# Optimization experiments

Hardware: AMD Instinct MI355X
Metric: run time of the kernel (lower is better)

Reference implementation:

```python
import jax, jax.numpy as jnp
import numpy as np

B, T, K_LAB = 32, 2048, 256
MASK = 1.0  # scalar mask blend coefficient from __init__ (1.0 = no padding)


def setup_inputs() -> dict:
    key = jax.random.key(0)
    k1, k2, k3 = jax.random.split(key, 3)
    y_pred = jax.random.normal(k1, (B, T, K_LAB), dtype=jnp.float32)  # emissions
    labels = jax.random.randint(k2, (B, T), 0, K_LAB, dtype=jnp.int32)  # gold tag ids
    # crf_trans weight, keras 'uniform' initializer ~ U(-0.05, 0.05)
    trans = jax.random.uniform(k3, (K_LAB, K_LAB), dtype=jnp.float32, minval=-0.05, maxval=0.05)
    return {"y_pred": y_pred, "trans": trans, "labels": labels}


def reference(y_pred, trans, labels):
    K = y_pred.shape[-1]
    y_true = jax.nn.one_hot(labels, K, dtype=y_pred.dtype)  # [B,T,K]

    # ---- path_score (unnormalized log prob of gold path) ----
    point_score = jnp.sum(y_pred * y_true, axis=(1, 2))[:, None]  # [B,1]
    # original materializes [B,T-1,K,K]; einsum computes the same contraction
    trans_score = jnp.einsum('bti,ij,btj->b', y_true[:, :-1], trans, y_true[:, 1:])[:, None]
    path_score = point_score + trans_score  # [B,1]

    # ---- log partition via forward algorithm (log-sum-exp semiring scan) ----
    init = y_pred[:, 0]  # [B,K]

    def step(state, x_t):
        # state: [B,K] alpha_{t-1};  x_t: [B,K] emissions at t
        new = jax.nn.logsumexp(state[:, :, None] + trans[None, :, :], axis=1) + x_t
        new = MASK * new + (1.0 - MASK) * state  # mask blend (identity for MASK=1)
        return new, None

    xs = jnp.swapaxes(y_pred[:, 1:], 0, 1)  # [T-1,B,K]
    final, _ = jax.lax.scan(step, init, xs)
    log_norm = jax.nn.logsumexp(final, axis=1, keepdims=True)  # [B,1]

    return log_norm - path_score  # [B,1] negative log-likelihood
```

## Files before the change

### kernel.cpp

```cpp
#include <hip/hip_runtime.h>

#define B_N 32
#define T_N 2048
#define K_N 256

typedef _Float16 f16x8 __attribute__((ext_vector_type(8)));
typedef float f32x4 __attribute__((ext_vector_type(4)));

#define LN2x5 3.46573590280f
#define C_ALL 7097.82712893f

__global__ __launch_bounds__(256) void k_rowmax(const float* __restrict__ y,
                                                float* __restrict__ mx) {
  int row = blockIdx.x * 4 + (threadIdx.x >> 6);
  int l = threadIdx.x & 63;
  const float4* p = (const float4*)(y + (size_t)row * K_N);
  float4 v = p[l];
  float m = fmaxf(fmaxf(v.x, v.y), fmaxf(v.z, v.w));
#pragma unroll
  for (int s = 1; s < 64; s <<= 1) m = fmaxf(m, __shfl_xor(m, s));
  if (l == 0) mx[row] = m;
}

__global__ __launch_bounds__(256) void k_expT(const float* __restrict__ trans,
                                              _Float16* __restrict__ ET) {
  int i = blockIdx.x;
  int j = threadIdx.x;
  ET[j * K_N + i] = (_Float16)__expf(trans[i * K_N + j]);
}

__global__ __launch_bounds__(256) void k_scores(
    const float* __restrict__ y, const int* __restrict__ lab,
    const float* __restrict__ trans, const float* __restrict__ mx,
    float* __restrict__ smx, float* __restrict__ path) {
  const int b = blockIdx.x;
  const int tid = threadIdx.x;
  float s_mx = 0.f, s_pt = 0.f, s_tr = 0.f;
  for (int t = tid; t < T_N; t += 256) {
    s_mx += mx[b * T_N + t];
    int lt = lab[b * T_N + t];
    s_pt += y[((size_t)b * T_N + t) * K_N + lt];
    if (t < T_N - 1) {
      int lnx = lab[b * T_N + t + 1];
      s_tr += trans[lt * K_N + lnx];
    }
  }
#pragma unroll
  for (int s = 1; s < 64; s <<= 1) {
    s_mx += __shfl_xor(s_mx, s);
    s_pt += __shfl_xor(s_pt, s);
    s_tr += __shfl_xor(s_tr, s);
  }
  __shared__ float r0[4], r1[4], r2[4];
  int w = tid >> 6, l = tid & 63;
  if (l == 0) { r0[w] = s_mx; r1[w] = s_pt; r2[w] = s_tr; }
  __syncthreads();
  if (tid == 0) {
    smx[b] = r0[0] + r0[1] + r0[2] + r0[3];
    path[b] = (r1[0] + r1[1] + r1[2] + r1[3]) + (r2[0] + r2[1] + r2[2] + r2[3]);
  }
}

__global__ __launch_bounds__(256, 1) void k_crf(
    const float* __restrict__ y, const _Float16* __restrict__ ET,
    const float* __restrict__ mx, const float* __restrict__ smx,
    const float* __restrict__ path, float* __restrict__ out) {
  const int b = blockIdx.x;
  const int tid = threadIdx.x;
  const int w = tid >> 6;
  const int l = tid & 63;
  const int lr = l & 15;
  const int lg = (l >> 4) & 3;

  alignas(16) __shared__ _Float16 vbuf[2][K_N];
  alignas(16) __shared__ float red[4];

  const float* __restrict__ yb = y + (size_t)b * T_N * K_N + w * 64 + lr;
  const float* __restrict__ mxb = mx + b * T_N;

  f16x8 E0[8], E1[8], E2[8], E3[8];
  {
    const f16x8* ETv = (const f16x8*)ET;
#pragma unroll
    for (int kt = 0; kt < 8; ++kt) {
      E0[kt] = ETv[(w * 64 + 0 * 16 + lr) * 32 + kt * 4 + lg];
      E1[kt] = ETv[(w * 64 + 1 * 16 + lr) * 32 + kt * 4 + lg];
      E2[kt] = ETv[(w * 64 + 2 * 16 + lr) * 32 + kt * 4 + lg];
      E3[kt] = ETv[(w * 64 + 3 * 16 + lr) * 32 + kt * 4 + lg];
    }
  }

  {
    float m0 = mxb[0];
    float yv = y[(size_t)b * T_N * K_N + w * 64 + lg * 16 + lr];
    vbuf[0][w * 64 + lg * 16 + lr] = (_Float16)__expf(yv - m0 - LN2x5);
  }

  float ys[4][4];
  float mxs[4];
#define PREF(P, TT) { int tp_ = (TT); tp_ = tp_ > (T_N - 1) ? (T_N - 1) : tp_; \
    const float* yp_ = yb + (size_t)tp_ * K_N;                                 \
    ys[P][0] = yp_[0];  ys[P][1] = yp_[16];                                    \
    ys[P][2] = yp_[32]; ys[P][3] = yp_[48];                                    \
    mxs[P] = mxb[tp_]; }

  PREF(0, 1) PREF(1, 2) PREF(2, 3) PREF(3, 4)

  float Cn = 0.0f;
  float wv0 = 0.f, wv1 = 0.f, wv2 = 0.f, wv3 = 0.f;

#define BARRIER asm volatile("s_waitcnt lgkmcnt(0)\ns_barrier" ::: "memory");

  BARRIER

#define STEP(TT, P, RB, WB, RENORM, APPLY, DO_STORE, DO_PREF, DO_BAR) {        \
    const f16x8* vv_ = (const f16x8*)&vbuf[RB][0];                             \
    f16x8 A_[8];                                                               \
    _Pragma("unroll")                                                          \
    for (int kt = 0; kt < 8; ++kt) A_[kt] = vv_[kt * 4 + lg];                  \
    float bias_ = mxs[P] + LN2x5;                                              \
    if (APPLY) {                                                               \
      f32x4 rv_ = *(const f32x4*)red;                                          \
      float mR_ = fmaxf(fmaxf(rv_[0], rv_[1]), fmaxf(rv_[2], rv_[3]));         \
      float lm_ = __logf(mR_);                                                 \
      Cn += lm_; bias_ += lm_;                                                 \
    }                                                                          \
    float e0_ = __expf(ys[P][0] - bias_);                                      \
    float e1_ = __expf(ys[P][1] - bias_);                                      \
    float e2_ = __expf(ys[P][2] - bias_);                                      \
    float e3_ = __expf(ys[P][3] - bias_);                                      \
    if (DO_PREF) PREF(P, (TT) + 4)                                             \
    f32x4 a0_ = {0.f, 0.f, 0.f, 0.f};                                          \
    f32x4 a1_ = a0_, a2_ = a0_, a3_ = a0_;                                     \
    _Pragma("unroll")                                                          \
    for (int kt = 0; kt < 8; ++kt) {                                           \
      a0_ = __builtin_amdgcn_mfma_f32_16x16x32_f16(A_[kt], E0[kt], a0_, 0, 0, 0); \
      a1_ = __builtin_amdgcn_mfma_f32_16x16x32_f16(A_[kt], E1[kt], a1_, 0, 0, 0); \
      a2_ = __builtin_amdgcn_mfma_f32_16x16x32_f16(A_[kt], E2[kt], a2_, 0, 0, 0); \
      a3_ = __builtin_amdgcn_mfma_f32_16x16x32_f16(A_[kt], E3[kt], a3_, 0, 0, 0); \
    }                                                                          \
    wv0 = a0_[0] * e0_; wv1 = a1_[0] * e1_;                                    \
    wv2 = a2_[0] * e2_; wv3 = a3_[0] * e3_;                                    \
    if (RENORM) {                                                              \
      float ml_ = fmaxf(fmaxf(wv0, wv1), fmaxf(wv2, wv3));                     \
      ml_ = fmaxf(ml_, __shfl_xor(ml_, 1));                                    \
      ml_ = fmaxf(ml_, __shfl_xor(ml_, 2));                                    \
      ml_ = fmaxf(ml_, __shfl_xor(ml_, 4));                                    \
      ml_ = fmaxf(ml_, __shfl_xor(ml_, 8));                                    \
      if (l == 0) red[w] = ml_;                                                \
    }                                                                          \
    if (DO_STORE) {                                                            \
      float sv_ = lg == 0 ? wv0 : lg == 1 ? wv1 : lg == 2 ? wv2 : wv3;         \
      vbuf[WB][w * 64 + lg * 16 + lr] = (_Float16)sv_;                         \
    }                                                                          \
    if (DO_BAR) BARRIER                                                        \
  }

  STEP(1, 0, 0, 1, 0, 0, 1, 1, 1)
  STEP(2, 1, 1, 0, 0, 0, 1, 1, 1)
  STEP(3, 2, 0, 1, 0, 0, 1, 1, 1)
  STEP(4, 3, 1, 0, 1, 0, 1, 1, 1)

#pragma unroll 1
  for (int t0 = 5; t0 <= T_N - 7; t0 += 4) {
    STEP(t0,     0, 0, 1, 0, 1, 1, 1, 1)
    STEP(t0 + 1, 1, 1, 0, 0, 0, 1, 1, 1)
    STEP(t0 + 2, 2, 0, 1, 0, 0, 1, 1, 1)
    STEP(t0 + 3, 3, 1, 0, 1, 0, 1, 1, 1)
  }

  STEP(2045, 0, 0, 1, 0, 1, 1, 0, 1)
  STEP(2046, 1, 1, 0, 0, 0, 1, 0, 1)
  STEP(2047, 2, 0, 1, 0, 0, 0, 0, 0)

  float s = wv0 + wv1 + wv2 + wv3;
  s += __shfl_xor(s, 1);
  s += __shfl_xor(s, 2);
  s += __shfl_xor(s, 4);
  s += __shfl_xor(s, 8);
  if (l == 0) red[w] = s;
  BARRIER
  if (tid == 0) {
    float S = red[0] + red[1] + red[2] + red[3];
    out[b] = __logf(S) + Cn + smx[b] + C_ALL - path[b];
  }
}

extern "C" void kernel_launch(void* const* d_in, const int* in_sizes, int n_in,
                              void* d_out, int out_size, void* d_ws, size_t ws_size,
                              hipStream_t stream) {
  const float* y = (const float*)d_in[0];
  const float* trans = (const float*)d_in[1];
  const int* lab = (const int*)d_in[2];
  float* out = (float*)d_out;

  float* mx = (float*)d_ws;
  _Float16* ET = (_Float16*)((char*)d_ws + (size_t)B_N * T_N * 4);
  float* smx = (float*)((char*)d_ws + (size_t)B_N * T_N * 4 + (size_t)K_N * K_N * 2);
  float* path = smx + B_N;

  k_rowmax<<<dim3(B_N * T_N / 4), dim3(256), 0, stream>>>(y, mx);
  k_expT<<<dim3(K_N), dim3(K_N), 0, stream>>>(trans, ET);
  k_scores<<<dim3(B_N), dim3(256), 0, stream>>>(y, lab, trans, mx, smx, path);
  k_crf<<<dim3(B_N), dim3(256), 0, stream>>>(y, ET, mx, smx, path, out);
}
```

Before: 1.134 ms.

## Use FP8 scaled MFMA with exp(trans)-1 decomposition and per-step sum normalization

The forward recursion now runs in FP8. The transition matrix is stored as exp(trans)-1 in FP8 and the state vector is kept in FP8 in shared memory, so each 16-column tile needs only two 16x16x128 f8f6f4 MFMAs instead of eight f16 MFMAs. The dominant 1 term is added back exactly through the previous-step sum (Sp + a), which preserves accuracy for small transition values. Renormalisation moves from a periodic max to a per-step sum with a log every step, which adds a shuffle reduction and a logf to every iteration of the serial critical path.

```diff
diff --git a/kernel.cpp b/kernel.cpp
--- a/kernel.cpp
+++ b/kernel.cpp
@@ -4,11 +4,11 @@
 #define T_N 2048
 #define K_N 256
 
-typedef _Float16 f16x8 __attribute__((ext_vector_type(8)));
 typedef float f32x4 __attribute__((ext_vector_type(4)));
+typedef int i32x8 __attribute__((ext_vector_type(8)));
 
-#define LN2x5 3.46573590280f
-#define C_ALL 7097.82712893f
+#define MFMA8(A, B, C) \
+  __builtin_amdgcn_mfma_scale_f32_16x16x128_f8f6f4((A), (B), (C), 0, 0, 0, 0x7F7F7F7F, 0, 0x7F7F7F7F)
 
 __global__ __launch_bounds__(256) void k_rowmax(const float* __restrict__ y,
                                                 float* __restrict__ mx) {
@@ -22,11 +22,13 @@
   if (l == 0) mx[row] = m;
 }
 
-__global__ __launch_bounds__(256) void k_expT(const float* __restrict__ trans,
-                                              _Float16* __restrict__ ET) {
-  int i = blockIdx.x;
-  int j = threadIdx.x;
-  ET[j * K_N + i] = (_Float16)__expf(trans[i * K_N + j]);
+__global__ __launch_bounds__(256) void k_g8(const float* __restrict__ trans,
+                                            unsigned char* __restrict__ GT) {
+  int j = blockIdx.x;
+  int i = threadIdx.x;
+  float g = __expf(trans[i * K_N + j]) - 1.0f;
+  int pk = __builtin_amdgcn_cvt_pk_fp8_f32(g, 0.f, 0, false);
+  GT[j * K_N + i] = (unsigned char)(pk & 0xff);
 }
 
 __global__ __launch_bounds__(256) void k_scores(
@@ -62,7 +64,7 @@
 }
 
 __global__ __launch_bounds__(256, 1) void k_crf(
-    const float* __restrict__ y, const _Float16* __restrict__ ET,
+    const float* __restrict__ y, const unsigned char* __restrict__ GT,
     const float* __restrict__ mx, const float* __restrict__ smx,
     const float* __restrict__ path, float* __restrict__ out) {
   const int b = blockIdx.x;
@@ -72,28 +74,29 @@
   const int lr = l & 15;
   const int lg = (l >> 4) & 3;
 
-  alignas(16) __shared__ _Float16 vbuf[2][K_N];
-  alignas(16) __shared__ float red[4];
+  alignas(64) __shared__ unsigned char vbuf8[2][K_N];
+  alignas(16) __shared__ float red2[2][4];
 
   const float* __restrict__ yb = y + (size_t)b * T_N * K_N + w * 64 + lr;
   const float* __restrict__ mxb = mx + b * T_N;
 
-  f16x8 E0[8], E1[8], E2[8], E3[8];
-  {
-    const f16x8* ETv = (const f16x8*)ET;
+  i32x8 Bf[4][2];
 #pragma unroll
-    for (int kt = 0; kt < 8; ++kt) {
-      E0[kt] = ETv[(w * 64 + 0 * 16 + lr) * 32 + kt * 4 + lg];
-      E1[kt] = ETv[(w * 64 + 1 * 16 + lr) * 32 + kt * 4 + lg];
-      E2[kt] = ETv[(w * 64 + 2 * 16 + lr) * 32 + kt * 4 + lg];
-      E3[kt] = ETv[(w * 64 + 3 * 16 + lr) * 32 + kt * 4 + lg];
-    }
+  for (int tt = 0; tt < 4; ++tt) {
+#pragma unroll
+    for (int h = 0; h < 2; ++h)
+      Bf[tt][h] = *(const i32x8*)(GT + (size_t)(w * 64 + tt * 16 + lr) * K_N + h * 128 + lg * 32);
   }
 
   {
-    float m0 = mxb[0];
-    float yv = y[(size_t)b * T_N * K_N + w * 64 + lg * 16 + lr];
-    vbuf[0][w * 64 + lg * 16 + lr] = (_Float16)__expf(yv - m0 - LN2x5);
+    int c0 = w * 64 + lg * 16 + lr;
+    float v0 = __expf(y[(size_t)b * T_N * K_N + c0] - mxb[0]);
+    int pk = __builtin_amdgcn_cvt_pk_fp8_f32(v0, 0.f, 0, false);
+    vbuf8[0][c0] = (unsigned char)(pk & 0xff);
+    float ps = v0;
+#pragma unroll
+    for (int s = 1; s < 64; s <<= 1) ps += __shfl_xor(ps, s);
+    if (l == 0) red2[0][w] = ps;
   }
 
   float ys[4][4];
@@ -113,76 +116,56 @@
 
   BARRIER
 
-#define STEP(TT, P, RB, WB, RENORM, APPLY, DO_STORE, DO_PREF, DO_BAR) {        \
-    const f16x8* vv_ = (const f16x8*)&vbuf[RB][0];                             \
-    f16x8 A_[8];                                                               \
-    _Pragma("unroll")                                                          \
-    for (int kt = 0; kt < 8; ++kt) A_[kt] = vv_[kt * 4 + lg];                  \
-    float bias_ = mxs[P] + LN2x5;                                              \
-    if (APPLY) {                                                               \
-      f32x4 rv_ = *(const f32x4*)red;                                          \
-      float mR_ = fmaxf(fmaxf(rv_[0], rv_[1]), fmaxf(rv_[2], rv_[3]));         \
-      float lm_ = __logf(mR_);                                                 \
-      Cn += lm_; bias_ += lm_;                                                 \
-    }                                                                          \
+#define STEP(TT, P, RB, WB, DO_PREF) {                                         \
+    f32x4 r_ = *(const f32x4*)(&red2[((TT) - 1) & 1][0]);                      \
+    i32x8 A0_ = *(const i32x8*)(&vbuf8[RB][lg * 32]);                          \
+    i32x8 A1_ = *(const i32x8*)(&vbuf8[RB][128 + lg * 32]);                    \
+    float Sp_ = (r_[0] + r_[1]) + (r_[2] + r_[3]);                             \
+    float ls_ = __logf(Sp_);                                                   \
+    float bias_ = mxs[P] + ls_;                                                \
     float e0_ = __expf(ys[P][0] - bias_);                                      \
     float e1_ = __expf(ys[P][1] - bias_);                                      \
     float e2_ = __expf(ys[P][2] - bias_);                                      \
     float e3_ = __expf(ys[P][3] - bias_);                                      \
     if (DO_PREF) PREF(P, (TT) + 4)                                             \
-    f32x4 a0_ = {0.f, 0.f, 0.f, 0.f};                                          \
-    f32x4 a1_ = a0_, a2_ = a0_, a3_ = a0_;                                     \
-    _Pragma("unroll")                                                          \
-    for (int kt = 0; kt < 8; ++kt) {                                           \
-      a0_ = __builtin_amdgcn_mfma_f32_16x16x32_f16(A_[kt], E0[kt], a0_, 0, 0, 0); \
-      a1_ = __builtin_amdgcn_mfma_f32_16x16x32_f16(A_[kt], E1[kt], a1_, 0, 0, 0); \
-      a2_ = __builtin_amdgcn_mfma_f32_16x16x32_f16(A_[kt], E2[kt], a2_, 0, 0, 0); \
-      a3_ = __builtin_amdgcn_mfma_f32_16x16x32_f16(A_[kt], E3[kt], a3_, 0, 0, 0); \
+    f32x4 z_ = {0.f, 0.f, 0.f, 0.f};                                           \
+    f32x4 a0_ = MFMA8(A1_, Bf[0][1], MFMA8(A0_, Bf[0][0], z_));                \
+    f32x4 a1_ = MFMA8(A1_, Bf[1][1], MFMA8(A0_, Bf[1][0], z_));                \
+    f32x4 a2_ = MFMA8(A1_, Bf[2][1], MFMA8(A0_, Bf[2][0], z_));                \
+    f32x4 a3_ = MFMA8(A1_, Bf[3][1], MFMA8(A0_, Bf[3][0], z_));                \
+    wv0 = (Sp_ + a0_[0]) * e0_;                                                \
+    wv1 = (Sp_ + a1_[0]) * e1_;                                                \
+    wv2 = (Sp_ + a2_[0]) * e2_;                                                \
+    wv3 = (Sp_ + a3_[0]) * e3_;                                                \
+    Cn += ls_;                                                                 \
+    float ps_ = (wv0 + wv1) + (wv2 + wv3);                                     \
+    ps_ += __shfl_xor(ps_, 1);                                                 \
+    ps_ += __shfl_xor(ps_, 2);                                                 \
+    ps_ += __shfl_xor(ps_, 4);                                                 \
+    ps_ += __shfl_xor(ps_, 8);                                                 \
+    if (l == 0) red2[(TT) & 1][w] = ps_;                                       \
+    {                                                                          \
+      float sv_ = lg == 0 ? wv0 : lg == 1 ? wv1 : lg == 2 ? wv2 : wv3;         \
+      int pk_ = __builtin_amdgcn_cvt_pk_fp8_f32(sv_, 0.f, 0, false);           \
+      vbuf8[WB][w * 64 + lg * 16 + lr] = (unsigned char)(pk_ & 0xff);          \
     }                                                                          \
-    wv0 = a0_[0] * e0_; wv1 = a1_[0] * e1_;                                    \
-    wv2 = a2_[0] * e2_; wv3 = a3_[0] * e3_;                                    \
-    if (RENORM) {                                                              \
-      float ml_ = fmaxf(fmaxf(wv0, wv1), fmaxf(wv2, wv3));                     \
-      ml_ = fmaxf(ml_, __shfl_xor(ml_, 1));                                    \
-      ml_ = fmaxf(ml_, __shfl_xor(ml_, 2));                                    \
-      ml_ = fmaxf(ml_, __shfl_xor(ml_, 4));                                    \
-      ml_ = fmaxf(ml_, __shfl_xor(ml_, 8));                                    \
-      if (l == 0) red[w] = ml_;                                                \
-    }                                                                          \
-    if (DO_STORE) {                                                            \
-      float sv_ = lg == 0 ? wv0 : lg == 1 ? wv1 : lg == 2 ? wv2 : wv3;         \
-      vbuf[WB][w * 64 + lg * 16 + lr] = (_Float16)sv_;                         \
-    }                                                                          \
-    if (DO_BAR) BARRIER                                                        \
+    BARRIER                                                                    \
   }
 
-  STEP(1, 0, 0, 1, 0, 0, 1, 1, 1)
-  STEP(2, 1, 1, 0, 0, 0, 1, 1, 1)
-  STEP(3, 2, 0, 1, 0, 0, 1, 1, 1)
-  STEP(4, 3, 1, 0, 1, 0, 1, 1, 1)
+#pragma unroll 1
+  for (int t0 = 1; t0 <= T_N - 7; t0 += 4) {
+    STEP(t0,     0, 0, 1, 1)
+    STEP(t0 + 1, 1, 1, 0, 1)
+    STEP(t0 + 2, 2, 0, 1, 1)
+    STEP(t0 + 3, 3, 1, 0, 1)
+  }
+  STEP(2045, 0, 0, 1, 0)
+  STEP(2046, 1, 1, 0, 0)
+  STEP(2047, 2, 0, 1, 0)
 
-#pragma unroll 1
-  for (int t0 = 5; t0 <= T_N - 7; t0 += 4) {
-    STEP(t0,     0, 0, 1, 0, 1, 1, 1, 1)
-    STEP(t0 + 1, 1, 1, 0, 0, 0, 1, 1, 1)
-    STEP(t0 + 2, 2, 0, 1, 0, 0, 1, 1, 1)
-    STEP(t0 + 3, 3, 1, 0, 1, 0, 1, 1, 1)
-  }
-
-  STEP(2045, 0, 0, 1, 0, 1, 1, 0, 1)
-  STEP(2046, 1, 1, 0, 0, 0, 1, 0, 1)
-  STEP(2047, 2, 0, 1, 0, 0, 0, 0, 0)
-
-  float s = wv0 + wv1 + wv2 + wv3;
-  s += __shfl_xor(s, 1);
-  s += __shfl_xor(s, 2);
-  s += __shfl_xor(s, 4);
-  s += __shfl_xor(s, 8);
-  if (l == 0) red[w] = s;
-  BARRIER
   if (tid == 0) {
-    float S = red[0] + red[1] + red[2] + red[3];
-    out[b] = __logf(S) + Cn + smx[b] + C_ALL - path[b];
+    float S = (red2[1][0] + red2[1][1]) + (red2[1][2] + red2[1][3]);
+    out[b] = __logf(S) + Cn + smx[b] - path[b];
   }
 }
 
@@ -195,12 +178,12 @@
   float* out = (float*)d_out;
 
   float* mx = (float*)d_ws;
-  _Float16* ET = (_Float16*)((char*)d_ws + (size_t)B_N * T_N * 4);
-  float* smx = (float*)((char*)d_ws + (size_t)B_N * T_N * 4 + (size_t)K_N * K_N * 2);
+  unsigned char* GT = (unsigned char*)d_ws + (size_t)B_N * T_N * 4;
+  float* smx = (float*)((char*)d_ws + (size_t)B_N * T_N * 4 + (size_t)K_N * K_N);
   float* path = smx + B_N;
 
   k_rowmax<<<dim3(B_N * T_N / 4), dim3(256), 0, stream>>>(y, mx);
-  k_expT<<<dim3(K_N), dim3(K_N), 0, stream>>>(trans, ET);
+  k_g8<<<dim3(K_N), dim3(256), 0, stream>>>(trans, GT);
   k_scores<<<dim3(B_N), dim3(256), 0, stream>>>(y, lab, trans, mx, smx, path);
-  k_crf<<<dim3(B_N), dim3(256), 0, stream>>>(y, ET, mx, smx, path, out);
+  k_crf<<<dim3(B_N), dim3(256), 0, stream>>>(y, GT, mx, smx, path, out);
 }
```

Result: no change. 1.134 ms (-0.0%).
